# Kernel tuning notes

Hardware: AMD Instinct MI355X
Metric: run time of the kernel (lower is better)

## Reference

```python
import jax, jax.numpy as jnp
import numpy as np
from jax import lax

B, T, F_DIM, E, H, L = 128, 160, 512, 64, 1024, 2
IN0 = F_DIM + E  # LSTM layer-0 input size (feat + target embedding)


def setup_inputs() -> dict:
    key = jax.random.key(0)
    ks = jax.random.split(key, 20)
    s_in0 = 1.0 / np.sqrt(IN0)
    s_h = 1.0 / np.sqrt(H)
    inp = {
        "feat": jax.random.normal(ks[0], (B, T, F_DIM), jnp.float32),
        "embedded_labels": jax.random.normal(ks[1], (B, T, E), jnp.float32),
        "mask": jax.random.bernoulli(ks[2], 0.3, (B, T)),
        # LSTM layer 0 (input IN0 -> H), gate order i,f,g,o as in torch
        "W_ih0": jax.random.normal(ks[3], (4 * H, IN0), jnp.float32) * s_in0,
        "W_hh0": jax.random.normal(ks[4], (4 * H, H), jnp.float32) * s_h,
        "b_ih0": jax.random.normal(ks[5], (4 * H,), jnp.float32) * s_h,
        "b_hh0": jax.random.normal(ks[6], (4 * H,), jnp.float32) * s_h,
        # LSTM layer 1 (H -> H)
        "W_ih1": jax.random.normal(ks[7], (4 * H, H), jnp.float32) * s_h,
        "W_hh1": jax.random.normal(ks[8], (4 * H, H), jnp.float32) * s_h,
        "b_ih1": jax.random.normal(ks[9], (4 * H,), jnp.float32) * s_h,
        "b_hh1": jax.random.normal(ks[10], (4 * H,), jnp.float32) * s_h,
        # target embedding: mu [B,1] @ W_tgt [1,E] + b_tgt
        "W_tgt": jax.random.normal(ks[11], (1, E), jnp.float32),
        "b_tgt": jax.random.normal(ks[12], (E,), jnp.float32) * 0.1,
        # mu / sigma projections from flattened hidden [B, H*L]
        "mu_w": jax.random.normal(ks[13], (H * L, 1), jnp.float32) * (1.0 / np.sqrt(H * L)),
        "mu_b": jnp.zeros((1,), jnp.float32),
        "sig_w": jax.random.normal(ks[14], (H * L, 1), jnp.float32) * (1.0 / np.sqrt(H * L)),
        "sig_b": jnp.zeros((1,), jnp.float32),
    }
    return inp


def _lstm_cell(x, h, c, W_ih, W_hh, b_ih, b_hh):
    g = x @ W_ih.T + b_ih + h @ W_hh.T + b_hh  # [B, 4H]
    gi, gf, gg, go = jnp.split(g, 4, axis=-1)
    c = jax.nn.sigmoid(gf) * c + jax.nn.sigmoid(gi) * jnp.tanh(gg)
    h = jax.nn.sigmoid(go) * jnp.tanh(c)
    return h, c


def reference(feat, embedded_labels, mask,
              W_ih0, W_hh0, b_ih0, b_hh0,
              W_ih1, W_hh1, b_ih1, b_hh1,
              W_tgt, b_tgt, mu_w, mu_b, sig_w, sig_b):
    Bq, Tq, _ = feat.shape
    Hq = W_hh0.shape[1]

    def step(carry, xs):
        h0, c0, h1, c1, mu = carry
        x_t, lab_t, m_t, idx = xs
        mu_embed = mu @ W_tgt + b_tgt  # [B, E]
        # i==0 always uses embedded_labels; otherwise where(mask, mu_embed, label)
        use_mu = (idx > 0) & m_t[:, None]
        lab = jnp.where(use_mu, mu_embed, lab_t)
        x = jnp.concatenate([x_t, lab], axis=-1)  # [B, IN0]
        h0, c0 = _lstm_cell(x, h0, c0, W_ih0, W_hh0, b_ih0, b_hh0)
        h1, c1 = _lstm_cell(h0, h1, c1, W_ih1, W_hh1, b_ih1, b_hh1)
        # torch: hidden[0].permute(1,2,0).view(B, H*L)
        hp = jnp.stack([h0, h1], axis=0).transpose(1, 2, 0).reshape(Bq, -1)
        mu = hp @ mu_w + mu_b  # [B, 1]
        sig = jax.nn.softplus(hp @ sig_w + sig_b)  # [B, 1]
        return (h0, c0, h1, c1, mu), (mu[:, 0], sig[:, 0])

    z = jnp.zeros((Bq, Hq), feat.dtype)
    init = (z, z, z, z, jnp.zeros((Bq, 1), feat.dtype))
    xs = (feat.transpose(1, 0, 2), embedded_labels.transpose(1, 0, 2),
          mask.T, jnp.arange(Tq))
    _, (mus, sigs) = lax.scan(step, init, xs)
    # [T,B] -> [B,T]; DeepAR stacks (mu, sigma) on last axis
    return jnp.stack((mus.T, sigs.T), axis=-1)  # [B, T, 2]
```

## Files before the change

kernel.cpp:

```cpp
#include <hip/hip_runtime.h>


#define B_   128
#define T_   160
#define FD   512
#define E_   64
#define H_   1024
#define NT   512
#define NBLK 256
#define CH0  100
#define CH1  128
#define HT_ELEMS (64 * 4 * 512)

typedef unsigned short u16;
typedef unsigned long long u64;
typedef __attribute__((ext_vector_type(8))) short bf16x8;
typedef __attribute__((ext_vector_type(16))) float f32x16;

__device__ __forceinline__ bf16x8 ld8(const u16* p) {
    return *reinterpret_cast<const bf16x8*>(p);
}
__device__ __forceinline__ bf16x8 ld8c(const u16* p) {
    u64* q = (u64*)p;
    union { u64 v[2]; bf16x8 f; } u_;
    u_.v[0] = __hip_atomic_load(q + 0, __ATOMIC_RELAXED, __HIP_MEMORY_SCOPE_AGENT);
    u_.v[1] = __hip_atomic_load(q + 1, __ATOMIC_RELAXED, __HIP_MEMORY_SCOPE_AGENT);
    return u_.f;
}
__device__ __forceinline__ float4 ld4f(const float* p) {
    u64* q = (u64*)p;
    union { u64 v[2]; float4 f; } u_;
    u_.v[0] = __hip_atomic_load(q + 0, __ATOMIC_RELAXED, __HIP_MEMORY_SCOPE_AGENT);
    u_.v[1] = __hip_atomic_load(q + 1, __ATOMIC_RELAXED, __HIP_MEMORY_SCOPE_AGENT);
    return u_.f;
}
__device__ __forceinline__ f32x16 mfma32(bf16x8 a, bf16x8 b, f32x16 c) {
    return __builtin_amdgcn_mfma_f32_32x32x16_bf16(a, b, c, 0, 0, 0);
}
__device__ __forceinline__ u16 f2bf(float x) {
    unsigned u = __float_as_uint(x);
    u += 0x7FFFu + ((u >> 16) & 1u);
    return (u16)(u >> 16);
}
__device__ __forceinline__ float sigm(float x)  { return 1.f / (1.f + __expf(-x)); }
__device__ __forceinline__ float tanh_(float x) { return 1.f - 2.f / (__expf(2.f * x) + 1.f); }
__device__ __forceinline__ float softp(float x) { return x > 20.f ? x : log1pf(__expf(x)); }

__device__ __forceinline__ void st_u32(unsigned* p, unsigned v) {
    __hip_atomic_store(p, v, __ATOMIC_RELAXED, __HIP_MEMORY_SCOPE_AGENT);
}
__device__ __forceinline__ void st_f32(float* p, float v) {
    __hip_atomic_store(p, v, __ATOMIC_RELAXED, __HIP_MEMORY_SCOPE_AGENT);
}

__device__ __forceinline__ void gbar(unsigned* actr, unsigned* rel, int blk, unsigned phase) {
    __syncthreads();
    if (threadIdx.x == 0) {
        __hip_atomic_fetch_add(&actr[(blk & 7) * 32], 1u,
                               __ATOMIC_RELAXED, __HIP_MEMORY_SCOPE_AGENT);
        if (blk == 0) {
            for (;;) {
                unsigned s = 0;
                #pragma unroll
                for (int i = 0; i < 8; ++i)
                    s += __hip_atomic_load(&actr[i * 32], __ATOMIC_RELAXED,
                                           __HIP_MEMORY_SCOPE_AGENT);
                if (s >= (unsigned)NBLK * phase) break;
                __builtin_amdgcn_s_sleep(2);
            }
            __hip_atomic_store(rel, phase, __ATOMIC_RELAXED, __HIP_MEMORY_SCOPE_AGENT);
        } else {
            while (__hip_atomic_load(rel, __ATOMIC_RELAXED, __HIP_MEMORY_SCOPE_AGENT) < phase)
                __builtin_amdgcn_s_sleep(2);
        }
    }
    __atomic_signal_fence(__ATOMIC_ACQUIRE);
    __syncthreads();
}


__global__ void detect_mask(const unsigned* __restrict__ m, int* __restrict__ flags) {
    int i = blockIdx.x * 256 + threadIdx.x;
    unsigned w = m[i];
    if (w > 1u) atomicOr(&flags[0], 1);
    if (w != 0u && w != 0x3F800000u) atomicOr(&flags[1], 1);
}

__global__ void featconv(const float* __restrict__ feat, u16* __restrict__ fb2) {
    int i = blockIdx.x * 256 + threadIdx.x;
    int t = i >> 14;
    int u = i & 16383;
    int c = u >> 9;
    int r = u & 511;
    int mm = r >> 7;
    int l  = (r >> 1) & 63;
    int jj = r & 1;
    int b = mm * 32 + (l & 31);
    int k = c * 16 + (l >> 5) * 8 + jj * 4;
    float4 v = reinterpret_cast<const float4*>(feat)[((size_t)b * T_ + t) * 128 + (k >> 2)];
    ushort4 o = make_ushort4(f2bf(v.x), f2bf(v.y), f2bf(v.z), f2bf(v.w));
    reinterpret_cast<ushort4*>(fb2)[((((size_t)t * 32 + c) * 4 + mm) * 512 + l * 8 + jj * 4) >> 2] = o;
}


struct SM0 {
    u16   bw[CH0 * 512];
    float gtb[4224];
    float mu_s[128];
    float uu[32], vv[32], bias[32];
    float mwv[8], swv[8];
    unsigned char msk[128];
};
struct SM1 {
    u16   bw[CH1 * 512];
    float gtb[4224];
    float bias[32];
    float mwv[8], swv[8];
};
union SMU { SM0 a; SM1 b; };

__global__ void __launch_bounds__(NT, 2) persist(
    const u16* __restrict__ fb2, const float* __restrict__ emb,
    const void* __restrict__ mask, const int* __restrict__ flags,
    const float* __restrict__ Wih0, const float* __restrict__ Whh0,
    const float* __restrict__ bih0, const float* __restrict__ bhh0,
    const float* __restrict__ Wih1, const float* __restrict__ Whh1,
    const float* __restrict__ bih1, const float* __restrict__ bhh1,
    const float* __restrict__ Wtgt, const float* __restrict__ btgt,
    const float* __restrict__ muw, const float* __restrict__ mubp,
    const float* __restrict__ sgw, const float* __restrict__ sgbp,
    u16* __restrict__ h0T, u16* __restrict__ h1T,
    float* __restrict__ muacc, float* __restrict__ sgacc,
    unsigned* __restrict__ actr, unsigned* __restrict__ relf,
    float* __restrict__ out)
{
    __shared__ SMU smu;
    const int tid  = threadIdx.x;
    const int blk  = blockIdx.x;
    const bool isL0 = blk < 128;
    const int g    = isL0 ? blk : blk - 128;
    const int wv   = tid >> 6;
    const int m    = wv & 3;
    const int s    = wv >> 2;
    const int lane = tid & 63;
    const int l31  = lane & 31;

    const float mub_r = mubp[0], sgb_r = sgbp[0];

    if (isL0) {
        SM0& s0 = smu.a;
        for (int i = tid; i < CH0 * 512; i += NT) {
            int ch = i >> 9, r = i & 511, l = r >> 3, jj = r & 7;
            int pc = l & 31;
            int kk = ch * 16 + (l >> 5) * 8 + jj;
            int q = pc & 3, j = pc >> 2;
            int row = q * H_ + g * 8 + j;
            float v = (kk < 576) ? Wih0[row * 576 + kk]
                                 : Whh0[(size_t)row * H_ + (kk - 576)];
            s0.bw[i] = f2bf(v);
        }
        if (tid < 32) {
            int pc = tid, q = pc & 3, j = pc >> 2;
            int row = q * H_ + g * 8 + j;
            s0.bias[pc] = bih0[row] + bhh0[row];
            float su = 0.f, sv = 0.f;
            for (int e = 0; e < 64; ++e) {
                float wl = Wih0[row * 576 + 512 + e];
                su += Wtgt[e] * wl;
                sv += btgt[e] * wl;
            }
            s0.uu[pc] = su; s0.vv[pc] = sv;
        }
        if (tid < 8) {
            int h = g * 8 + tid;
            s0.mwv[tid] = muw[2 * h]; s0.swv[tid] = sgw[2 * h];
        }
    } else {
        SM1& s1 = smu.b;
        for (int i = tid; i < CH1 * 512; i += NT) {
            int ch = i >> 9, r = i & 511, l = r >> 3, jj = r & 7;
            int pc = l & 31;
            int kk = ch * 16 + (l >> 5) * 8 + jj;
            int q = pc & 3, j = pc >> 2;
            int row = q * H_ + g * 8 + j;
            float v = (kk < 1024) ? Wih1[(size_t)row * H_ + kk]
                                  : Whh1[(size_t)row * H_ + (kk - 1024)];
            s1.bw[i] = f2bf(v);
        }
        if (tid < 32) {
            int pc = tid, q = pc & 3, j = pc >> 2;
            int row = q * H_ + g * 8 + j;
            s1.bias[pc] = bih1[row] + bhh1[row];
        }
        if (tid < 8) {
            int h = g * 8 + tid;
            s1.mwv[tid] = muw[2 * h + 1]; s1.swv[tid] = sgw[2 * h + 1];
        }
    }
    const int nonbin = flags[0], nonfl = flags[1];
    __syncthreads();

    float creg0 = 0.f, creg1 = 0.f;
    f32x16 acc;
    #pragma unroll
    for (int r = 0; r < 16; ++r) acc[r] = 0.f;

    auto reduce_gates = [&](float* g_) {
        if (s == 1) {
            #pragma unroll
            for (int r = 0; r < 16; ++r) g_[r * 256 + m * 64 + lane] = acc[r];
        }
        __syncthreads();
        f32x16 tot;
        if (s == 0) {
            #pragma unroll
            for (int r = 0; r < 16; ++r) tot[r] = acc[r] + g_[r * 256 + m * 64 + lane];
        }
        __syncthreads();
        if (s == 0) {
            #pragma unroll
            for (int r = 0; r < 16; ++r) {
                int row = m * 32 + (r & 3) + 8 * (r >> 2) + 4 * (lane >> 5);
                g_[row * 33 + l31] = tot[r];
            }
        }
        #pragma unroll
        for (int r = 0; r < 16; ++r) acc[r] = 0.f;
    };

    auto hgemm = [&](const u16* hp, const u16* bwb) {
        bf16x8 areg[32];
        #pragma unroll
        for (int c = 0; c < 32; ++c) {
            int ch = s * 32 + c;
            areg[c] = ld8c(hp + ((size_t)ch * 4 + m) * 512 + lane * 8);
        }
        #pragma unroll
        for (int c = 0; c < 32; ++c) {
            int ch = s * 32 + c;
            bf16x8 b = *(const bf16x8*)&bwb[ch * 512 + lane * 8];
            acc = mfma32(areg[c], b, acc);
        }
    };

    auto featlab = [&](int t1, bool use_mask) {
        SM0& s0 = smu.a;
        const int bq = m * 32 + l31;
        bool um = false;
        if (use_mask && s == 1) {
            int mi = bq * T_ + t1;
            um = !nonbin ? (reinterpret_cast<const int*>(mask)[mi] != 0)
               : !nonfl  ? (reinterpret_cast<const float*>(mask)[mi] != 0.f)
                         : (reinterpret_cast<const unsigned char*>(mask)[mi] != 0);
        }
        #pragma unroll 6
        for (int c = 0; c < 18; ++c) {
            int ch = s * 18 + c;
            bf16x8 a;
            if (ch < 32) {
                a = ld8(fb2 + (((size_t)t1 * 32 + ch) * 4 + m) * 512 + lane * 8);
            } else {
                const float* ep = &emb[((size_t)bq * T_ + t1) * 64
                                       + (ch - 32) * 16 + (lane >> 5) * 8];
                float4 v0 = *reinterpret_cast<const float4*>(ep);
                float4 v1 = *reinterpret_cast<const float4*>(ep + 4);
                if (um) { v0.x=v0.y=v0.z=v0.w=0.f; v1.x=v1.y=v1.z=v1.w=0.f; }
                a[0] = (short)f2bf(v0.x); a[1] = (short)f2bf(v0.y);
                a[2] = (short)f2bf(v0.z); a[3] = (short)f2bf(v0.w);
                a[4] = (short)f2bf(v1.x); a[5] = (short)f2bf(v1.y);
                a[6] = (short)f2bf(v1.z); a[7] = (short)f2bf(v1.w);
            }
            bf16x8 b = *(const bf16x8*)&s0.bw[ch * 512 + lane * 8];
            acc = mfma32(a, b, acc);
        }
    };

    if (isL0) {
        featlab(0, false);
        reduce_gates(smu.a.gtb);
    }

    unsigned bc = 0;
    for (int t = 0; t < T_; ++t) {
        const int pcur = t & 1, pprev = pcur ^ 1;

        if (isL0) {
            SM0& s0 = smu.a;
            if (t > 0 && tid < 128) {
                float4 x = ld4f(&muacc[(pprev * 128 + tid) * 8]);
                float4 y = ld4f(&muacc[(pprev * 128 + tid) * 8 + 4]);
                s0.mu_s[tid] = (x.x + x.y) + (x.z + x.w) + (y.x + y.y) + (y.z + y.w) + mub_r;
                int mi = tid * T_ + t;
                bool um = !nonbin ? (reinterpret_cast<const int*>(mask)[mi] != 0)
                        : !nonfl  ? (reinterpret_cast<const float*>(mask)[mi] != 0.f)
                                  : (reinterpret_cast<const unsigned char*>(mask)[mi] != 0);
                s0.msk[tid] = um ? 1 : 0;
            }
            __syncthreads();
            if (t > 0 && tid == 0) {
                float4 x = ld4f(&sgacc[(pprev * 128 + g) * 8]);
                float4 y = ld4f(&sgacc[(pprev * 128 + g) * 8 + 4]);
                float sg = (x.x + x.y) + (x.z + x.w) + (y.x + y.y) + (y.z + y.w) + sgb_r;
                out[((size_t)g * T_ + (t - 1)) * 2 + 0] = s0.mu_s[g];
                out[((size_t)g * T_ + (t - 1)) * 2 + 1] = softp(sg);
            }
            u16* hw = h0T + (size_t)pcur * HT_ELEMS;
            const int c_ = g >> 1, half = g & 1;
            #pragma unroll
            for (int p = 0; p < 2; ++p) {
                int id = tid + p * NT;
                int b = id >> 3, j = id & 7;
                float gi = s0.gtb[b * 33 + 4 * j + 0] + s0.bias[4 * j + 0];
                float gf = s0.gtb[b * 33 + 4 * j + 1] + s0.bias[4 * j + 1];
                float gg = s0.gtb[b * 33 + 4 * j + 2] + s0.bias[4 * j + 2];
                float go = s0.gtb[b * 33 + 4 * j + 3] + s0.bias[4 * j + 3];
                if (t > 0 && s0.msk[b]) {
                    float mu = s0.mu_s[b];
                    gi += mu * s0.uu[4 * j + 0] + s0.vv[4 * j + 0];
                    gf += mu * s0.uu[4 * j + 1] + s0.vv[4 * j + 1];
                    gg += mu * s0.uu[4 * j + 2] + s0.vv[4 * j + 2];
                    go += mu * s0.uu[4 * j + 3] + s0.vv[4 * j + 3];
                }
                float cold = (p == 0) ? creg0 : creg1;
                float cn = sigm(gf) * cold + sigm(gi) * tanh_(gg);
                float hn = sigm(go) * tanh_(cn);
                if (p == 0) creg0 = cn; else creg1 = cn;
                unsigned hv = f2bf(hn);
                unsigned other = (unsigned)__shfl_xor((int)hv, 1);
                if ((j & 1) == 0) {
                    int l = half * 32 + (b & 31), mb = b >> 5;
                    st_u32(reinterpret_cast<unsigned*>(hw + ((size_t)(c_ * 4 + mb) * 512 + l * 8 + j)),
                           hv | (other << 16));
                }
                float pmu = hn * s0.mwv[j], psg = hn * s0.swv[j];
                pmu += __shfl_xor(pmu, 1); pmu += __shfl_xor(pmu, 2); pmu += __shfl_xor(pmu, 4);
                psg += __shfl_xor(psg, 1); psg += __shfl_xor(psg, 2); psg += __shfl_xor(psg, 4);
                if (j == 0) {
                    atomicAdd(&muacc[(pcur * 128 + b) * 8 + (g & 7)], pmu);
                    atomicAdd(&sgacc[(pcur * 128 + b) * 8 + (g & 7)], psg);
                }
            }
            if (t + 1 < T_) featlab(t + 1, true);
        } else {
            SM1& s1 = smu.b;
            if (t > 0) {
                hgemm(h1T + (size_t)pprev * HT_ELEMS, &s1.bw[64 * 512]);
            }
        }
        gbar(actr, relf, blk, ++bc);

        if (isL0) {
            SM0& s0 = smu.a;
            if (t + 1 < T_) {
                hgemm(h0T + (size_t)pcur * HT_ELEMS, &s0.bw[36 * 512]);
                reduce_gates(s0.gtb);
            }
        } else {
            SM1& s1 = smu.b;
            if (tid < 8) {
                st_f32(&muacc[(pprev * 128 + g) * 8 + tid], 0.f);
                st_f32(&sgacc[(pprev * 128 + g) * 8 + tid], 0.f);
            }
            hgemm(h0T + (size_t)pcur * HT_ELEMS, &s1.bw[0]);
            reduce_gates(s1.gtb);
            __syncthreads();
            u16* hw = h1T + (size_t)pcur * HT_ELEMS;
            const int c_ = g >> 1, half = g & 1;
            #pragma unroll
            for (int p = 0; p < 2; ++p) {
                int id = tid + p * NT;
                int b = id >> 3, j = id & 7;
                float gi = s1.gtb[b * 33 + 4 * j + 0] + s1.bias[4 * j + 0];
                float gf = s1.gtb[b * 33 + 4 * j + 1] + s1.bias[4 * j + 1];
                float gg = s1.gtb[b * 33 + 4 * j + 2] + s1.bias[4 * j + 2];
                float go = s1.gtb[b * 33 + 4 * j + 3] + s1.bias[4 * j + 3];
                float cold = (p == 0) ? creg0 : creg1;
                float cn = sigm(gf) * cold + sigm(gi) * tanh_(gg);
                float hn = sigm(go) * tanh_(cn);
                if (p == 0) creg0 = cn; else creg1 = cn;
                unsigned hv = f2bf(hn);
                unsigned other = (unsigned)__shfl_xor((int)hv, 1);
                if ((j & 1) == 0) {
                    int l = half * 32 + (b & 31), mb = b >> 5;
                    st_u32(reinterpret_cast<unsigned*>(hw + ((size_t)(c_ * 4 + mb) * 512 + l * 8 + j)),
                           hv | (other << 16));
                }
                float pmu = hn * s1.mwv[j], psg = hn * s1.swv[j];
                pmu += __shfl_xor(pmu, 1); pmu += __shfl_xor(pmu, 2); pmu += __shfl_xor(pmu, 4);
                psg += __shfl_xor(psg, 1); psg += __shfl_xor(psg, 2); psg += __shfl_xor(psg, 4);
                if (j == 0) {
                    atomicAdd(&muacc[(pcur * 128 + b) * 8 + (g & 7)], pmu);
                    atomicAdd(&sgacc[(pcur * 128 + b) * 8 + (g & 7)], psg);
                }
            }
        }
        gbar(actr, relf, blk, ++bc);
    }

    if (isL0 && tid == 0) {
        float4 x = ld4f(&muacc[(1 * 128 + g) * 8]);
        float4 y = ld4f(&muacc[(1 * 128 + g) * 8 + 4]);
        float mu = (x.x + x.y) + (x.z + x.w) + (y.x + y.y) + (y.z + y.w) + mub_r;
        float4 z = ld4f(&sgacc[(1 * 128 + g) * 8]);
        float4 u2 = ld4f(&sgacc[(1 * 128 + g) * 8 + 4]);
        float sg = (z.x + z.y) + (z.z + z.w) + (u2.x + u2.y) + (u2.z + u2.w) + sgb_r;
        out[((size_t)g * T_ + (T_ - 1)) * 2 + 0] = mu;
        out[((size_t)g * T_ + (T_ - 1)) * 2 + 1] = softp(sg);
    }
}


extern "C" void kernel_launch(void* const* d_in, const int* in_sizes, int n_in,
                              void* d_out, int out_size, void* d_ws, size_t ws_size,
                              hipStream_t stream) {
    const float* feat = (const float*)d_in[0];
    const float* emb  = (const float*)d_in[1];
    const void*  mask = d_in[2];
    const float* Wih0 = (const float*)d_in[3];
    const float* Whh0 = (const float*)d_in[4];
    const float* bih0 = (const float*)d_in[5];
    const float* bhh0 = (const float*)d_in[6];
    const float* Wih1 = (const float*)d_in[7];
    const float* Whh1 = (const float*)d_in[8];
    const float* bih1 = (const float*)d_in[9];
    const float* bhh1 = (const float*)d_in[10];
    const float* Wtgt = (const float*)d_in[11];
    const float* btgt = (const float*)d_in[12];
    const float* muw  = (const float*)d_in[13];
    const float* mub  = (const float*)d_in[14];
    const float* sgw  = (const float*)d_in[15];
    const float* sgb  = (const float*)d_in[16];
    float* out = (float*)d_out;
    char* ws = (char*)d_ws;
    (void)in_sizes; (void)n_in; (void)out_size; (void)ws_size;

    size_t off = 0;
    auto alloc = [&](size_t bytes) {
        size_t o = off;
        off = (off + bytes + 255) & ~(size_t)255;
        return o;
    };
    size_t o_flags = alloc(256);
    size_t o_actr  = alloc(8 * 32 * 4);
    size_t o_rel   = alloc(256);
    size_t o_muacc = alloc((size_t)2 * 128 * 8 * 4);
    size_t o_sgacc = alloc((size_t)2 * 128 * 8 * 4);
    size_t zero_end = off;
    size_t o_h0    = alloc((size_t)2 * HT_ELEMS * 2);
    size_t o_h1    = alloc((size_t)2 * HT_ELEMS * 2);
    size_t o_fb2   = alloc((size_t)T_ * 32 * 4 * 512 * 2);

    int*      flags = (int*)(ws + o_flags);
    unsigned* actr  = (unsigned*)(ws + o_actr);
    unsigned* relf  = (unsigned*)(ws + o_rel);
    float*    muacc = (float*)(ws + o_muacc);
    float*    sgacc = (float*)(ws + o_sgacc);
    u16*      h0    = (u16*)(ws + o_h0);
    u16*      h1    = (u16*)(ws + o_h1);
    u16*      fb2   = (u16*)(ws + o_fb2);

    hipMemsetAsync(ws, 0, zero_end, stream);
    detect_mask<<<20, 256, 0, stream>>>((const unsigned*)mask, flags);
    featconv<<<10240, 256, 0, stream>>>(feat, fb2);

    persist<<<NBLK, NT, 0, stream>>>(
        fb2, emb, mask, flags,
        Wih0, Whh0, bih0, bhh0,
        Wih1, Whh1, bih1, bhh1,
        Wtgt, btgt, muw, mub, sgw, sgb,
        h0, h1, muacc, sgacc, actr, relf, out);
}
```

Baseline: 3.657 ms.

## Replace global barriers with per-layer producer/consumer flag counters

Swaps the two grid-wide barriers per timestep, each funnelled through block 0's release flag, for two sets of split arrival counters: one that layer-0 blocks bump after writing h0, and one that layer-1 blocks bump after writing h1. Each block waits only on the counters it depends on, and the step is reordered so layer-0 computes its next hgemm right after h0 is ready while layer-1 overlaps its h0 gemm with waiting for h1. This removes the serial release hop and lets the two layers run skewed instead of in lockstep. The trade-off is more polling traffic on the counters and subtler memory-ordering requirements for the muacc/sgacc reset and the mu feedback.

```diff
diff --git a/kernel.cpp b/kernel.cpp
--- a/kernel.cpp
+++ b/kernel.cpp
@@ -53,29 +53,27 @@
     __hip_atomic_store(p, v, __ATOMIC_RELAXED, __HIP_MEMORY_SCOPE_AGENT);
 }
 
-__device__ __forceinline__ void gbar(unsigned* actr, unsigned* rel, int blk, unsigned phase) {
-    __syncthreads();
+__device__ __forceinline__ void waitf(unsigned* lines, unsigned target) {
     if (threadIdx.x == 0) {
-        __hip_atomic_fetch_add(&actr[(blk & 7) * 32], 1u,
-                               __ATOMIC_RELAXED, __HIP_MEMORY_SCOPE_AGENT);
-        if (blk == 0) {
-            for (;;) {
-                unsigned s = 0;
-                #pragma unroll
-                for (int i = 0; i < 8; ++i)
-                    s += __hip_atomic_load(&actr[i * 32], __ATOMIC_RELAXED,
-                                           __HIP_MEMORY_SCOPE_AGENT);
-                if (s >= (unsigned)NBLK * phase) break;
-                __builtin_amdgcn_s_sleep(2);
-            }
-            __hip_atomic_store(rel, phase, __ATOMIC_RELAXED, __HIP_MEMORY_SCOPE_AGENT);
-        } else {
-            while (__hip_atomic_load(rel, __ATOMIC_RELAXED, __HIP_MEMORY_SCOPE_AGENT) < phase)
-                __builtin_amdgcn_s_sleep(2);
+        for (;;) {
+            unsigned s = 0;
+            #pragma unroll
+            for (int i = 0; i < 8; ++i)
+                s += __hip_atomic_load(&lines[i * 32], __ATOMIC_RELAXED,
+                                       __HIP_MEMORY_SCOPE_AGENT);
+            if (s >= target) break;
+            __builtin_amdgcn_s_sleep(1);
         }
     }
     __atomic_signal_fence(__ATOMIC_ACQUIRE);
     __syncthreads();
+}
+__device__ __forceinline__ void arrivef(unsigned* lines, int g) {
+    __builtin_amdgcn_s_waitcnt(0);
+    __syncthreads();
+    if (threadIdx.x == 0)
+        __hip_atomic_fetch_add(&lines[(g & 7) * 32], 1u,
+                               __ATOMIC_RELAXED, __HIP_MEMORY_SCOPE_AGENT);
 }
 
 
@@ -131,7 +129,7 @@
     const float* __restrict__ sgw, const float* __restrict__ sgbp,
     u16* __restrict__ h0T, u16* __restrict__ h1T,
     float* __restrict__ muacc, float* __restrict__ sgacc,
-    unsigned* __restrict__ actr, unsigned* __restrict__ relf,
+    unsigned* __restrict__ actr,
     float* __restrict__ out)
 {
     __shared__ SMU smu;
@@ -144,6 +142,9 @@
     const int s    = wv >> 2;
     const int lane = tid & 63;
     const int l31  = lane & 31;
+
+    unsigned* f0l = actr;
+    unsigned* f1l = actr + 8 * 32;
 
     const float mub_r = mubp[0], sgb_r = sgbp[0];
 
@@ -280,21 +281,23 @@
         reduce_gates(smu.a.gtb);
     }
 
-    unsigned bc = 0;
     for (int t = 0; t < T_; ++t) {
         const int pcur = t & 1, pprev = pcur ^ 1;
 
         if (isL0) {
             SM0& s0 = smu.a;
-            if (t > 0 && tid < 128) {
-                float4 x = ld4f(&muacc[(pprev * 128 + tid) * 8]);
-                float4 y = ld4f(&muacc[(pprev * 128 + tid) * 8 + 4]);
-                s0.mu_s[tid] = (x.x + x.y) + (x.z + x.w) + (y.x + y.y) + (y.z + y.w) + mub_r;
-                int mi = tid * T_ + t;
-                bool um = !nonbin ? (reinterpret_cast<const int*>(mask)[mi] != 0)
-                        : !nonfl  ? (reinterpret_cast<const float*>(mask)[mi] != 0.f)
-                                  : (reinterpret_cast<const unsigned char*>(mask)[mi] != 0);
-                s0.msk[tid] = um ? 1 : 0;
+            if (t > 0) {
+                waitf(f1l, 128u * (unsigned)t);
+                if (tid < 128) {
+                    float4 x = ld4f(&muacc[(pprev * 128 + tid) * 8]);
+                    float4 y = ld4f(&muacc[(pprev * 128 + tid) * 8 + 4]);
+                    s0.mu_s[tid] = (x.x + x.y) + (x.z + x.w) + (y.x + y.y) + (y.z + y.w) + mub_r;
+                    int mi = tid * T_ + t;
+                    bool um = !nonbin ? (reinterpret_cast<const int*>(mask)[mi] != 0)
+                            : !nonfl  ? (reinterpret_cast<const float*>(mask)[mi] != 0.f)
+                                      : (reinterpret_cast<const unsigned char*>(mask)[mi] != 0);
+                    s0.msk[tid] = um ? 1 : 0;
+                }
             }
             __syncthreads();
             if (t > 0 && tid == 0) {
@@ -340,28 +343,26 @@
                     atomicAdd(&sgacc[(pcur * 128 + b) * 8 + (g & 7)], psg);
                 }
             }
-            if (t + 1 < T_) featlab(t + 1, true);
+            arrivef(f0l, g);
+
+            if (t + 1 < T_) {
+                waitf(f0l, 128u * (unsigned)(t + 1));
+                hgemm(h0T + (size_t)pcur * HT_ELEMS, &s0.bw[36 * 512]);
+                featlab(t + 1, true);
+                reduce_gates(s0.gtb);
+            }
         } else {
             SM1& s1 = smu.b;
-            if (t > 0) {
-                hgemm(h1T + (size_t)pprev * HT_ELEMS, &s1.bw[64 * 512]);
-            }
-        }
-        gbar(actr, relf, blk, ++bc);
-
-        if (isL0) {
-            SM0& s0 = smu.a;
-            if (t + 1 < T_) {
-                hgemm(h0T + (size_t)pcur * HT_ELEMS, &s0.bw[36 * 512]);
-                reduce_gates(s0.gtb);
-            }
-        } else {
-            SM1& s1 = smu.b;
-            if (tid < 8) {
+            waitf(f0l, 128u * (unsigned)(t + 1));
+            if (t > 0 && tid < 8) {
                 st_f32(&muacc[(pprev * 128 + g) * 8 + tid], 0.f);
                 st_f32(&sgacc[(pprev * 128 + g) * 8 + tid], 0.f);
             }
             hgemm(h0T + (size_t)pcur * HT_ELEMS, &s1.bw[0]);
+            if (t > 0) {
+                waitf(f1l, 128u * (unsigned)t);
+                hgemm(h1T + (size_t)pprev * HT_ELEMS, &s1.bw[64 * 512]);
+            }
             reduce_gates(s1.gtb);
             __syncthreads();
             u16* hw = h1T + (size_t)pcur * HT_ELEMS;
@@ -393,19 +394,22 @@
                     atomicAdd(&sgacc[(pcur * 128 + b) * 8 + (g & 7)], psg);
                 }
             }
-        }
-        gbar(actr, relf, blk, ++bc);
+            arrivef(f1l, g);
+        }
     }
 
-    if (isL0 && tid == 0) {
-        float4 x = ld4f(&muacc[(1 * 128 + g) * 8]);
-        float4 y = ld4f(&muacc[(1 * 128 + g) * 8 + 4]);
-        float mu = (x.x + x.y) + (x.z + x.w) + (y.x + y.y) + (y.z + y.w) + mub_r;
-        float4 z = ld4f(&sgacc[(1 * 128 + g) * 8]);
-        float4 u2 = ld4f(&sgacc[(1 * 128 + g) * 8 + 4]);
-        float sg = (z.x + z.y) + (z.z + z.w) + (u2.x + u2.y) + (u2.z + u2.w) + sgb_r;
-        out[((size_t)g * T_ + (T_ - 1)) * 2 + 0] = mu;
-        out[((size_t)g * T_ + (T_ - 1)) * 2 + 1] = softp(sg);
+    if (isL0) {
+        waitf(f1l, 128u * (unsigned)T_);
+        if (tid == 0) {
+            float4 x = ld4f(&muacc[(1 * 128 + g) * 8]);
+            float4 y = ld4f(&muacc[(1 * 128 + g) * 8 + 4]);
+            float mu = (x.x + x.y) + (x.z + x.w) + (y.x + y.y) + (y.z + y.w) + mub_r;
+            float4 z = ld4f(&sgacc[(1 * 128 + g) * 8]);
+            float4 u2 = ld4f(&sgacc[(1 * 128 + g) * 8 + 4]);
+            float sg = (z.x + z.y) + (z.z + z.w) + (u2.x + u2.y) + (u2.z + u2.w) + sgb_r;
+            out[((size_t)g * T_ + (T_ - 1)) * 2 + 0] = mu;
+            out[((size_t)g * T_ + (T_ - 1)) * 2 + 1] = softp(sg);
+        }
     }
 }
 
@@ -441,8 +445,7 @@
         return o;
     };
     size_t o_flags = alloc(256);
-    size_t o_actr  = alloc(8 * 32 * 4);
-    size_t o_rel   = alloc(256);
+    size_t o_actr  = alloc(16 * 32 * 4);
     size_t o_muacc = alloc((size_t)2 * 128 * 8 * 4);
     size_t o_sgacc = alloc((size_t)2 * 128 * 8 * 4);
     size_t zero_end = off;
@@ -452,7 +455,6 @@
 
     int*      flags = (int*)(ws + o_flags);
     unsigned* actr  = (unsigned*)(ws + o_actr);
-    unsigned* relf  = (unsigned*)(ws + o_rel);
     float*    muacc = (float*)(ws + o_muacc);
     float*    sgacc = (float*)(ws + o_sgacc);
     u16*      h0    = (u16*)(ws + o_h0);
@@ -468,5 +470,5 @@
         Wih0, Whh0, bih0, bhh0,
         Wih1, Whh1, bih1, bhh1,
         Wtgt, btgt, muw, mub, sgw, sgb,
-        h0, h1, muacc, sgacc, actr, relf, out);
-}
+        h0, h1, muacc, sgacc, actr, out);
+}
```

Result: slower. 4.986 ms (+36.3%).
